# Kernel optimization log

Hardware: AMD Instinct MI355X
Metric: run time of the kernel (lower is better)

## Reference

```python
import jax, jax.numpy as jnp
import numpy as np

HW = 24       # image_size // patch_size
HEAD = 16     # vision num_attention_heads
B, T, C, H = 8, 8, 1024, 4096


def _sincos_1d(d, pos):
    omega = np.arange(d // 2, dtype=np.float32) / (d / 2.0)
    omega = 1.0 / 10000 ** omega
    out = np.einsum('m,d->md', pos.reshape(-1).astype(np.float32), omega)
    return np.concatenate([np.sin(out), np.cos(out)], axis=1)


def _pos_embed_3d(embed_dim, grid_size, t_size):
    ds = embed_dim // 4 * 3
    dt = embed_dim // 4
    gh = np.arange(grid_size, dtype=np.float32)
    grid = np.stack(np.meshgrid(gh, gh), axis=0).reshape(2, -1)  # (w, h) order as in source
    spatial = np.concatenate([_sincos_1d(ds // 2, grid[0]), _sincos_1d(ds // 2, grid[1])], axis=1)  # [g*g, ds]
    temporal = _sincos_1d(dt, np.arange(t_size, dtype=np.float32))  # [t, dt]
    spatial = np.repeat(spatial[np.newaxis], t_size, axis=0)                 # [t, g*g, ds]
    temporal = np.repeat(temporal[:, np.newaxis], grid_size ** 2, axis=1)    # [t, g*g, dt]
    emb = np.concatenate([temporal, spatial], axis=-1)
    return emb.reshape(1, t_size * grid_size ** 2, embed_dim).astype(np.float32)


def setup_inputs() -> dict:
    key = jax.random.key(0)
    k1, k2, k3 = jax.random.split(key, 3)
    x = jax.random.normal(k1, (B, T * HW * HW, C), dtype=jnp.float32)
    W1 = jax.random.normal(k2, (C, H), dtype=jnp.float32) * 0.02
    b1 = jnp.zeros((H,), jnp.float32)
    W2 = jax.random.normal(k3, (H, H), dtype=jnp.float32) * 0.02
    b2 = jnp.zeros((H,), jnp.float32)
    pos_embed = jnp.asarray(_pos_embed_3d(C, HW, T))
    return {"x": x, "pos_embed": pos_embed, "W1": W1, "b1": b1, "W2": W2, "b2": b2,
            "local_num_frames": T}


def _merge(x, unm_idx, src_idx, dst_idx):
    # ToMe merge: gather unmatched src tokens, scatter-add matched src into dst.
    src, dst = x[:, ::2], x[:, 1::2]
    unm = jnp.take_along_axis(src, unm_idx[:, :, None], axis=1)   # [b, t1-r, c]
    sel = jnp.take_along_axis(src, src_idx[:, :, None], axis=1)   # [b, r, c]
    dst = jax.vmap(lambda d, i, s: d.at[i].add(s))(dst, dst_idx, sel)
    return jnp.concatenate([unm, dst], axis=1)


def _merge_tokens(x, target, head):
    b, p, c = x.shape
    # static merge schedule (same logic as torch merge_tokens)
    rs, tmp = [], p
    while tmp != target:
        if tmp - target <= tmp // 2:
            rs.append(tmp - target)
            break
        rs.append(tmp // 2)
        tmp -= tmp // 2
    dim = c // head
    size = jnp.ones((b, p, 1), x.dtype)
    for r in rs:
        bb, pp, _ = x.shape
        # metric/index computation is under no_grad in the original
        metric = jax.lax.stop_gradient(x).reshape(bb, pp, head, dim).mean(2)
        metric = metric / jnp.linalg.norm(metric, axis=-1, keepdims=True)
        a_m, b_m = metric[:, ::2], metric[:, 1::2]
        scores = jnp.einsum('bic,bjc->bij', a_m, b_m)  # [b, ta, tb]
        node_max = scores.max(-1)
        node_idx = scores.argmax(-1)
        edge_idx = jnp.argsort(-node_max, axis=-1)      # descending
        unm_idx, src_idx = edge_idx[:, r:], edge_idx[:, :r]
        dst_idx = jnp.take_along_axis(node_idx, src_idx, axis=1)
        # weighted-average merge (merge_wavg)
        x = _merge(x * size, unm_idx, src_idx, dst_idx)
        size = _merge(size, unm_idx, src_idx, dst_idx)
        x = x / size
    return x


def reference(x, pos_embed, W1, b1, W2, b2, local_num_frames):
    x = x + pos_embed.astype(x.dtype)
    x = _merge_tokens(x, local_num_frames * 16, HEAD)
    h = jax.nn.gelu(x @ W1 + b1, approximate=False)  # nn.GELU() is exact erf gelu
    return h @ W2 + b2
```

## Files before the change

kernel.cpp:

```cpp
#include <hip/hip_runtime.h>
#include <hip/hip_bf16.h>
#include <math.h>
#include <stdint.h>

typedef unsigned short u16;
typedef __attribute__((ext_vector_type(8))) short short8;
typedef __attribute__((ext_vector_type(4))) float floatx4;

#define NB 8
#define P0 4608
#define C0 1024
#define H0 4096

__global__ void detect_mode_kernel(const uint32_t* __restrict__ pe_words, int* __restrict__ mode) {
  *mode = (pe_words[64] != 0u) ? 1 : 0;
}

__device__ __forceinline__ float load_in(const void* p, size_t idx, int mode) {
  if (mode) return __bfloat162float(((const __hip_bfloat16*)p)[idx]);
  return ((const float*)p)[idx];
}

__device__ __forceinline__ float4 load4(const void* p, size_t idx, int mode) {
  float4 r;
  if (mode) {
    ushort4 u = *(const ushort4*)((const u16*)p + idx);
    r.x = __bfloat162float(*(__hip_bfloat16*)&u.x);
    r.y = __bfloat162float(*(__hip_bfloat16*)&u.y);
    r.z = __bfloat162float(*(__hip_bfloat16*)&u.z);
    r.w = __bfloat162float(*(__hip_bfloat16*)&u.w);
  } else {
    r = *(const float4*)((const float*)p + idx);
  }
  return r;
}

__device__ __forceinline__ void write_hilo(u16* __restrict__ m2, size_t tok, int lane, float v) {
  __hip_bfloat16 hi = __float2bfloat16(v);
  float hif = __bfloat162float(hi);
  __hip_bfloat16 lo = __float2bfloat16(v - hif);
  m2[tok * 128 + lane] = *(u16*)&hi;
  m2[tok * 128 + 64 + lane] = *(u16*)&lo;
}

__global__ void metric_in_kernel(const void* __restrict__ x, const void* __restrict__ pos,
                                 const int* __restrict__ mode, u16* __restrict__ m2) {
  int tok = blockIdx.x * 4 + (threadIdx.x >> 6);
  int lane = threadIdx.x & 63;
  if (tok >= NB * P0) return;
  int b = tok / P0, t = tok - b * P0;
  int md = *mode;
  size_t xbase = ((size_t)b * P0 + t) * C0 + lane;
  size_t pbase = (size_t)t * C0 + lane;
  float s = 0.f;
  if (md) {
    const __hip_bfloat16* xp = (const __hip_bfloat16*)x + xbase;
    const __hip_bfloat16* pp = (const __hip_bfloat16*)pos + pbase;
#pragma unroll
    for (int h = 0; h < 16; ++h)
      s += __bfloat162float(xp[h * 64]) + __bfloat162float(pp[h * 64]);
  } else {
    const float* xp = (const float*)x + xbase;
    const float* pp = (const float*)pos + pbase;
#pragma unroll
    for (int h = 0; h < 16; ++h) s += xp[h * 64] + pp[h * 64];
  }
  s *= (1.f / 16.f);
  float sq = s * s;
#pragma unroll
  for (int off = 1; off < 64; off <<= 1) sq += __shfl_xor(sq, off, 64);
  write_hilo(m2, (size_t)tok, lane, s / sqrtf(sq));
}

__global__ __launch_bounds__(256) void score_mfma_kernel(const u16* __restrict__ M2,
                                                         int p, int p2, int jT2,
                                                         float* __restrict__ pm,
                                                         int* __restrict__ pi) {
  const int bi = blockIdx.x, ii = blockIdx.y, b = blockIdx.z;
  const int t = threadIdx.x, w = t >> 6, L = t & 63;
  const int wr = w >> 1, wc = w & 1;
  const int fr = L & 15, fo = (L >> 4) * 8;
  const u16* Mb = M2 + (size_t)b * p * 128;

  floatx4 acc[4][4];
#pragma unroll
  for (int mt = 0; mt < 4; ++mt)
#pragma unroll
    for (int nt = 0; nt < 4; ++nt) acc[mt][nt] = (floatx4){0.f, 0.f, 0.f, 0.f};

  const u16* arp[4];
  const u16* brp[4];
#pragma unroll
  for (int mt = 0; mt < 4; ++mt) {
    int i = ii * 128 + wr * 64 + mt * 16 + fr;
    int ta = 2 * i;
    if (ta > p - 2) ta = p - 2;
    arp[mt] = Mb + (size_t)ta * 128 + fo;
    int j = bi * 128 + wc * 64 + mt * 16 + fr;
    int tb = 2 * j + 1;
    if (tb > p - 1) tb = p - 1;
    brp[mt] = Mb + (size_t)tb * 128 + fo;
  }

#pragma unroll
  for (int ks = 0; ks < 2; ++ks) {
    short8 ah[4], al[4], bh[4], bl[4];
#pragma unroll
    for (int mt = 0; mt < 4; ++mt) {
      ah[mt] = *(const short8*)(arp[mt] + ks * 32);
      al[mt] = *(const short8*)(arp[mt] + ks * 32 + 64);
      bh[mt] = *(const short8*)(brp[mt] + ks * 32);
      bl[mt] = *(const short8*)(brp[mt] + ks * 32 + 64);
    }
#pragma unroll
    for (int mt = 0; mt < 4; ++mt)
#pragma unroll
      for (int nt = 0; nt < 4; ++nt) {
        acc[mt][nt] = __builtin_amdgcn_mfma_f32_16x16x32_bf16(ah[mt], bh[nt], acc[mt][nt], 0, 0, 0);
        acc[mt][nt] = __builtin_amdgcn_mfma_f32_16x16x32_bf16(ah[mt], bl[nt], acc[mt][nt], 0, 0, 0);
        acc[mt][nt] = __builtin_amdgcn_mfma_f32_16x16x32_bf16(al[mt], bh[nt], acc[mt][nt], 0, 0, 0);
        acc[mt][nt] = __builtin_amdgcn_mfma_f32_16x16x32_bf16(al[mt], bl[nt], acc[mt][nt], 0, 0, 0);
      }
  }

  const int gi4 = (L >> 4) * 4;
#pragma unroll
  for (int mt = 0; mt < 4; ++mt) {
#pragma unroll
    for (int reg = 0; reg < 4; ++reg) {
      int i = ii * 128 + wr * 64 + mt * 16 + gi4 + reg;
      float bm = -INFINITY;
      int bj = 0x7fffffff;
#pragma unroll
      for (int nt = 0; nt < 4; ++nt) {
        int j = bi * 128 + wc * 64 + nt * 16 + fr;
        float v = acc[mt][nt][reg];
        if (j < p2 && v > bm) { bm = v; bj = j; }
      }
#pragma unroll
      for (int mk = 1; mk < 16; mk <<= 1) {
        float om = __shfl_xor(bm, mk, 64);
        int oj = __shfl_xor(bj, mk, 64);
        if (om > bm || (om == bm && oj < bj)) { bm = om; bj = oj; }
      }
      if (fr == 0 && i < p2) {
        size_t o = ((size_t)b * 2304 + i) * jT2 + bi * 2 + wc;
        pm[o] = bm;
        pi[o] = bj;
      }
    }
  }
}

__global__ void argmax_combine_kernel(const float* __restrict__ pm, const int* __restrict__ pi,
                                      int p2, int jT, float* __restrict__ nmax,
                                      int* __restrict__ nidx, int* __restrict__ head,
                                      int* __restrict__ nxt) {
  int g = blockIdx.x * 256 + threadIdx.x;
  if (g >= NB * p2) return;
  int b = g / p2, i = g - b * p2;
  const float* r = pm + ((size_t)b * 2304 + i) * jT;
  const int* ri = pi + ((size_t)b * 2304 + i) * jT;
  float best = r[0];
  int bidx = ri[0];
  for (int k = 1; k < jT; ++k) {
    if (r[k] > best || (r[k] == best && ri[k] < bidx)) { best = r[k]; bidx = ri[k]; }
  }
  nmax[g] = best;
  nidx[g] = bidx;
  int d = bidx;
  if ((unsigned)d >= (unsigned)p2) d = 0;
  nxt[g] = atomicExch(&head[(size_t)b * p2 + d], i);
}

__global__ void init_heads_kernel(int* __restrict__ h, int n) {
  int g = blockIdx.x * 256 + threadIdx.x;
  if (g < n) h[g] = -1;
}

__global__ __launch_bounds__(256) void merge_gather_in(const void* __restrict__ x,
                                                       const void* __restrict__ pos,
                                                       const int* __restrict__ mode,
                                                       const int* __restrict__ head,
                                                       const int* __restrict__ nxt,
                                                       float* __restrict__ xo,
                                                       float* __restrict__ so, int p2,
                                                       u16* __restrict__ m2out) {
  int tj = blockIdx.x;
  int b = tj / p2, j = tj - b * p2;
  int c = threadIdx.x * 4;
  int md = *mode;
  __shared__ int sl[64];
  __shared__ int s_n, s_cur;
  __shared__ float mred[16][64];
  size_t xb = ((size_t)b * P0 + 2 * j + 1) * C0 + c;
  size_t pb = (size_t)(2 * j + 1) * C0 + c;
  float4 xa = load4(x, xb, md), pa = load4(pos, pb, md);
  float4 acc = {xa.x + pa.x, xa.y + pa.y, xa.z + pa.z, xa.w + pa.w};
  float cnt = 1.f;
  if (threadIdx.x == 0) s_cur = head[tj];
  __syncthreads();
  int cur = s_cur;
  while (cur != -1) {
    if (threadIdx.x == 0) {
      int n = 0, cc = cur;
      while (cc != -1 && n < 64) {
        sl[n++] = cc;
        cc = nxt[(size_t)b * p2 + cc];
      }
      s_n = n;
      s_cur = cc;
    }
    __syncthreads();
    int n = s_n;
    cur = s_cur;
    for (int k = 0; k < n; ++k) {
      int i = sl[k];
      size_t exb = ((size_t)b * P0 + 2 * i) * C0 + c;
      size_t epb = (size_t)(2 * i) * C0 + c;
      float4 ea = load4(x, exb, md), ep = load4(pos, epb, md);
      acc.x += ea.x + ep.x;
      acc.y += ea.y + ep.y;
      acc.z += ea.z + ep.z;
      acc.w += ea.w + ep.w;
      cnt += 1.f;
    }
    __syncthreads();
  }
  float inv = 1.f / cnt;
  float4 o = {acc.x * inv, acc.y * inv, acc.z * inv, acc.w * inv};
  *(float4*)(xo + (size_t)tj * C0 + c) = o;
  if (threadIdx.x == 0) so[tj] = cnt;
  {
    int hq = threadIdx.x >> 4, dq = (threadIdx.x & 15) * 4;
    mred[hq][dq + 0] = o.x;
    mred[hq][dq + 1] = o.y;
    mred[hq][dq + 2] = o.z;
    mred[hq][dq + 3] = o.w;
  }
  __syncthreads();
  if (threadIdx.x < 64) {
    float s = 0.f;
#pragma unroll
    for (int h = 0; h < 16; ++h) s += mred[h][threadIdx.x];
    s *= (1.f / 16.f);
    float sq = s * s;
#pragma unroll
    for (int off = 1; off < 64; off <<= 1) sq += __shfl_xor(sq, off, 64);
    write_hilo(m2out, (size_t)tj, threadIdx.x, s / sqrtf(sq));
  }
}

__global__ __launch_bounds__(256) void merge_gather_f(const float* __restrict__ xi,
                                                      const float* __restrict__ si,
                                                      const int* __restrict__ head,
                                                      const int* __restrict__ nxt,
                                                      float* __restrict__ xo,
                                                      float* __restrict__ so, int p, int p2,
                                                      u16* __restrict__ m2out) {
  int tj = blockIdx.x;
  int b = tj / p2, j = tj - b * p2;
  int c = threadIdx.x * 4;
  __shared__ int sl[64];
  __shared__ int s_n, s_cur;
  __shared__ float mred[16][64];
  float sz = si[(size_t)b * p + 2 * j + 1];
  float4 v = *(const float4*)(xi + ((size_t)b * p + 2 * j + 1) * C0 + c);
  float4 acc = {v.x * sz, v.y * sz, v.z * sz, v.w * sz};
  float ssum = sz;
  if (threadIdx.x == 0) s_cur = head[tj];
  __syncthreads();
  int cur = s_cur;
  while (cur != -1) {
    if (threadIdx.x == 0) {
      int n = 0, cc = cur;
      while (cc != -1 && n < 64) {
        sl[n++] = cc;
        cc = nxt[(size_t)b * p2 + cc];
      }
      s_n = n;
      s_cur = cc;
    }
    __syncthreads();
    int n = s_n;
    cur = s_cur;
    for (int k = 0; k < n; ++k) {
      int i = sl[k];
      float szi = si[(size_t)b * p + 2 * i];
      float4 e = *(const float4*)(xi + ((size_t)b * p + 2 * i) * C0 + c);
      acc.x += e.x * szi;
      acc.y += e.y * szi;
      acc.z += e.z * szi;
      acc.w += e.w * szi;
      ssum += szi;
    }
    __syncthreads();
  }
  float inv = 1.f / ssum;
  float4 o = {acc.x * inv, acc.y * inv, acc.z * inv, acc.w * inv};
  *(float4*)(xo + (size_t)tj * C0 + c) = o;
  if (threadIdx.x == 0) so[tj] = ssum;
  {
    int hq = threadIdx.x >> 4, dq = (threadIdx.x & 15) * 4;
    mred[hq][dq + 0] = o.x;
    mred[hq][dq + 1] = o.y;
    mred[hq][dq + 2] = o.z;
    mred[hq][dq + 3] = o.w;
  }
  __syncthreads();
  if (threadIdx.x < 64) {
    float s = 0.f;
#pragma unroll
    for (int h = 0; h < 16; ++h) s += mred[h][threadIdx.x];
    s *= (1.f / 16.f);
    float sq = s * s;
#pragma unroll
    for (int off = 1; off < 64; off <<= 1) sq += __shfl_xor(sq, off, 64);
    write_hilo(m2out, (size_t)tj, threadIdx.x, s / sqrtf(sq));
  }
}

__global__ void rank_kernel(const float* __restrict__ nmax, const int* __restrict__ nidx,
                            int* __restrict__ unm_map, int* __restrict__ src_ord,
                            int* __restrict__ src_dst) {
  int b = blockIdx.x;
  int i = threadIdx.x;
  __shared__ float v[72];
  __shared__ int nx[72];
  if (i < 72) { v[i] = nmax[b * 72 + i]; nx[i] = nidx[b * 72 + i]; }
  __syncthreads();
  if (i < 72) {
    float vi = v[i];
    int rank = 0;
    for (int k = 0; k < 72; ++k) {
      float vk = v[k];
      rank += (vk > vi) || (vk == vi && k < i);
    }
    if (rank < 16) {
      int d = nx[i];
      if ((unsigned)d >= 72u) d = 0;
      src_ord[b * 16 + rank] = i;
      src_dst[b * 16 + rank] = d;
    } else {
      unm_map[b * 56 + (rank - 16)] = i;
    }
  }
}

__global__ void final_init(const float* __restrict__ x5, const float* __restrict__ s5,
                           const int* __restrict__ unm_map, float* __restrict__ xf,
                           float* __restrict__ sf) {
  int bt = blockIdx.x;
  int b = bt >> 7, tk = bt & 127;
  int c = threadIdx.x * 4;
  float4 o;
  float szo;
  if (tk < 56) {
    int se = unm_map[b * 56 + tk];
    if ((unsigned)se >= 72u) se = 0;
    o = *(const float4*)(x5 + ((size_t)b * 144 + 2 * se) * C0 + c);
    szo = 1.f;
  } else {
    int j = tk - 56;
    float sz = s5[b * 144 + 2 * j + 1];
    float4 v = *(const float4*)(x5 + ((size_t)b * 144 + 2 * j + 1) * C0 + c);
    o.x = v.x * sz; o.y = v.y * sz; o.z = v.z * sz; o.w = v.w * sz;
    szo = sz;
  }
  *(float4*)(xf + (size_t)bt * C0 + c) = o;
  if (threadIdx.x == 0) sf[bt] = szo;
}

__global__ void final_scatter(const float* __restrict__ x5, const float* __restrict__ s5,
                              const int* __restrict__ src_ord, const int* __restrict__ src_dst,
                              float* __restrict__ xf, float* __restrict__ sf) {
  int bk = blockIdx.x;
  int b = bk >> 4, k = bk & 15;
  int c = threadIdx.x * 4;
  int st = src_ord[b * 16 + k], dst = src_dst[b * 16 + k];
  if ((unsigned)st >= 72u) st = 0;
  if ((unsigned)dst >= 72u) dst = 0;
  float sz = s5[b * 144 + 2 * st];
  float4 v = *(const float4*)(x5 + ((size_t)b * 144 + 2 * st) * C0 + c);
  float* out = xf + ((size_t)(b * 128 + 56 + dst)) * C0 + c;
  atomicAdd(out + 0, v.x * sz);
  atomicAdd(out + 1, v.y * sz);
  atomicAdd(out + 2, v.z * sz);
  atomicAdd(out + 3, v.w * sz);
  if (threadIdx.x == 0) atomicAdd(sf + b * 128 + 56 + dst, sz);
}

__global__ void final_div_cvt(const float* __restrict__ xf, const float* __restrict__ sf,
                              __hip_bfloat16* __restrict__ xb) {
  int bt = blockIdx.x;
  int c = threadIdx.x * 4;
  float sz = sf[bt];
  float4 v = *(const float4*)(xf + (size_t)bt * C0 + c);
  __hip_bfloat16* o = xb + (size_t)bt * C0 + c;
  o[0] = __float2bfloat16(v.x / sz);
  o[1] = __float2bfloat16(v.y / sz);
  o[2] = __float2bfloat16(v.z / sz);
  o[3] = __float2bfloat16(v.w / sz);
}

__global__ void transpose_in(const void* __restrict__ in, const int* __restrict__ mode,
                             u16* __restrict__ out, int K, int N) {
  __shared__ u16 tile[64][65];
  int n0 = blockIdx.x * 64, k0 = blockIdx.y * 64;
  int t = threadIdx.x;
  int md = *mode;
  int r = t >> 4, c4 = (t & 15) * 4;
  if (md) {
#pragma unroll
    for (int pass = 0; pass < 4; ++pass) {
      int row = r + pass * 16;
      ushort4 u = *(const ushort4*)((const u16*)in + (size_t)(k0 + row) * N + n0 + c4);
      tile[row][c4 + 0] = u.x;
      tile[row][c4 + 1] = u.y;
      tile[row][c4 + 2] = u.z;
      tile[row][c4 + 3] = u.w;
    }
  } else {
#pragma unroll
    for (int pass = 0; pass < 4; ++pass) {
      int row = r + pass * 16;
      float4 v = *(const float4*)((const float*)in + (size_t)(k0 + row) * N + n0 + c4);
      __hip_bfloat16 b0 = __float2bfloat16(v.x), b1 = __float2bfloat16(v.y);
      __hip_bfloat16 b2 = __float2bfloat16(v.z), b3 = __float2bfloat16(v.w);
      tile[row][c4 + 0] = *(u16*)&b0;
      tile[row][c4 + 1] = *(u16*)&b1;
      tile[row][c4 + 2] = *(u16*)&b2;
      tile[row][c4 + 3] = *(u16*)&b3;
    }
  }
  __syncthreads();
#pragma unroll
  for (int pass = 0; pass < 4; ++pass) {
    int row = r + pass * 16;
    ushort4 o;
    o.x = tile[c4][row]; o.y = tile[c4 + 1][row]; o.z = tile[c4 + 2][row]; o.w = tile[c4 + 3][row];
    *(ushort4*)(out + (size_t)(n0 + row) * K + k0 + c4) = o;
  }
}

#define GL2LDS(gp, lp)                                                                   \
  __builtin_amdgcn_global_load_lds((const __attribute__((address_space(1))) uint32_t*)(gp), \
                                   (__attribute__((address_space(3))) uint32_t*)(lp), 16, 0, 0)

__global__ __launch_bounds__(256, 2) void gemm_bt(const u16* __restrict__ A,
                                                  const u16* __restrict__ BT,
                                                  const void* __restrict__ bias,
                                                  const int* __restrict__ mode,
                                                  void* __restrict__ C, int M, int N,
                                                  int K, int act, int out_sel) {
  __shared__ __align__(16) u16 As[2 * 64 * 64];
  __shared__ __align__(16) u16 Bs[2 * 128 * 64];
  const int t = threadIdx.x, w = t >> 6, L = t & 63;
  const int m0 = blockIdx.y * 64, n0 = blockIdx.x * 128;
  const int wr = w >> 1, wc = w & 1;
  const int md = *mode;
  const int fr = L & 15;
  floatx4 acc[2][4];
#pragma unroll
  for (int a = 0; a < 2; ++a)
#pragma unroll
    for (int bb = 0; bb < 4; ++bb) acc[a][bb] = (floatx4){0.f, 0.f, 0.f, 0.f};

  auto stage = [&](int buf, int kk) {
#pragma unroll
    for (int q = 0; q < 2; ++q) {
      int g = q * 256 + t;
      int row = g >> 3, colg = (g & 7) ^ (row & 7);
      GL2LDS(A + (size_t)(m0 + row) * K + kk + colg * 8, As + buf * 4096 + g * 8);
    }
#pragma unroll
    for (int q = 0; q < 4; ++q) {
      int g = q * 256 + t;
      int row = g >> 3, colg = (g & 7) ^ (row & 7);
      GL2LDS(BT + (size_t)(n0 + row) * K + kk + colg * 8, Bs + buf * 8192 + g * 8);
    }
  };

  stage(0, 0);
  const int NT = K >> 6;
  int cur = 0;
  for (int it = 0; it < NT; ++it) {
    if (it + 1 < NT) {
      stage(cur ^ 1, (it + 1) << 6);
      asm volatile("s_waitcnt vmcnt(6)" ::: "memory");
    } else {
      asm volatile("s_waitcnt vmcnt(0)" ::: "memory");
    }
    __builtin_amdgcn_s_barrier();
    const u16* Ab = As + cur * 4096;
    const u16* Bb = Bs + cur * 8192;
    __builtin_amdgcn_s_setprio(1);
#pragma unroll
    for (int kh = 0; kh < 2; ++kh) {
      short8 af[2], bfr[4];
#pragma unroll
      for (int mt = 0; mt < 2; ++mt) {
        int ra = wr * 32 + mt * 16 + fr;
        int cg = (kh * 4 + (L >> 4)) ^ (ra & 7);
        af[mt] = *(const short8*)(Ab + ra * 64 + cg * 8);
      }
#pragma unroll
      for (int nt = 0; nt < 4; ++nt) {
        int rb = wc * 64 + nt * 16 + fr;
        int cg = (kh * 4 + (L >> 4)) ^ (rb & 7);
        bfr[nt] = *(const short8*)(Bb + rb * 64 + cg * 8);
      }
#pragma unroll
      for (int mt = 0; mt < 2; ++mt)
#pragma unroll
        for (int nt = 0; nt < 4; ++nt)
          acc[mt][nt] =
              __builtin_amdgcn_mfma_f32_16x16x32_bf16(af[mt], bfr[nt], acc[mt][nt], 0, 0, 0);
    }
    __builtin_amdgcn_s_setprio(0);
    __builtin_amdgcn_s_barrier();
    cur ^= 1;
  }
  const int gi4 = (L >> 4) * 4;
#pragma unroll
  for (int mt = 0; mt < 2; ++mt)
#pragma unroll
    for (int nt = 0; nt < 4; ++nt) {
      int n = n0 + wc * 64 + nt * 16 + fr;
      float bz = load_in(bias, n, md);
#pragma unroll
      for (int rr = 0; rr < 4; ++rr) {
        int m = m0 + wr * 32 + mt * 16 + gi4 + rr;
        float v = acc[mt][nt][rr] + bz;
        if (act) v = 0.5f * v * (1.f + erff(v * 0.70710678118654752f));
        size_t idx = (size_t)m * N + n;
        if (out_sel == 0 || md) {
          __hip_bfloat16 bv = __float2bfloat16(v);
          ((u16*)C)[idx] = *(u16*)&bv;
        } else {
          ((float*)C)[idx] = v;
        }
      }
    }
}

extern "C" void kernel_launch(void* const* d_in, const int* in_sizes, int n_in, void* d_out,
                              int out_size, void* d_ws, size_t ws_size, hipStream_t stream) {
  const void* x = d_in[0];
  const void* pe = d_in[1];
  const void* W1 = d_in[2];
  const void* b1 = d_in[3];
  const void* W2 = d_in[4];
  const void* b2 = d_in[5];

  char* base = (char*)d_ws;
  size_t off = 0;
  auto alloc = [&](size_t bytes) -> void* {
    void* p = base + off;
    off += (bytes + 255) & ~(size_t)255;
    return p;
  };
  int* mode = (int*)alloc(256);
  u16* m2 = (u16*)alloc((size_t)NB * 4608 * 128 * 2);
  float* pm = (float*)alloc((size_t)NB * 2304 * 36 * 4);
  int* pi = (int*)alloc((size_t)NB * 2304 * 36 * 4);
  float* nmax = (float*)alloc((size_t)NB * 2304 * 4);
  int* nidx = (int*)alloc((size_t)NB * 2304 * 4);
  float* bufA = (float*)alloc((size_t)NB * 2304 * C0 * 4);
  float* bufB = (float*)alloc((size_t)NB * 1152 * C0 * 4);
  float* s1 = (float*)alloc((size_t)NB * 2304 * 4);
  float* s2 = (float*)alloc((size_t)NB * 1152 * 4);
  float* s3 = (float*)alloc((size_t)NB * 576 * 4);
  float* s4 = (float*)alloc((size_t)NB * 288 * 4);
  float* s5 = (float*)alloc((size_t)NB * 144 * 4);
  float* sf = (float*)alloc((size_t)NB * 128 * 4);
  int* unm_map = (int*)alloc((size_t)NB * 56 * 4);
  int* src_ord = (int*)alloc((size_t)NB * 16 * 4);
  int* src_dst = (int*)alloc((size_t)NB * 16 * 4);
  u16* xfb = (u16*)alloc((size_t)NB * 128 * C0 * 2);
  u16* hbuf = (u16*)alloc((size_t)1024 * H0 * 2);
  u16* w1t = (u16*)alloc((size_t)H0 * C0 * 2);
  u16* w2t = (u16*)alloc((size_t)H0 * H0 * 2);
  int* heads = (int*)alloc((size_t)NB * 4536 * 4);
  int* nxt = (int*)alloc((size_t)NB * 2304 * 4);
  if (off > ws_size) return;

  int* h_it[6];
  h_it[0] = heads;
  h_it[1] = h_it[0] + NB * 2304;
  h_it[2] = h_it[1] + NB * 1152;
  h_it[3] = h_it[2] + NB * 576;
  h_it[4] = h_it[3] + NB * 288;
  h_it[5] = h_it[4] + NB * 144;

  float* x1 = bufA;
  float* x2 = bufB;
  float* x3 = bufA;
  float* x4 = bufB;
  float* x5 = bufA;
  float* xf = bufB;

  detect_mode_kernel<<<1, 1, 0, stream>>>((const uint32_t*)pe, mode);
  init_heads_kernel<<<(NB * 4536 + 255) / 256, 256, 0, stream>>>(heads, NB * 4536);

  transpose_in<<<dim3(4096 / 64, 1024 / 64), 256, 0, stream>>>(W1, mode, w1t, 1024, 4096);
  transpose_in<<<dim3(4096 / 64, 4096 / 64), 256, 0, stream>>>(W2, mode, w2t, 4096, 4096);

  metric_in_kernel<<<NB * P0 / 4, 256, 0, stream>>>(x, pe, mode, m2);
  score_mfma_kernel<<<dim3(18, 18, NB), 256, 0, stream>>>(m2, 4608, 2304, 36, pm, pi);
  argmax_combine_kernel<<<(NB * 2304 + 255) / 256, 256, 0, stream>>>(pm, pi, 2304, 36, nmax,
                                                                     nidx, h_it[0], nxt);
  merge_gather_in<<<NB * 2304, 256, 0, stream>>>(x, pe, mode, h_it[0], nxt, x1, s1, 2304, m2);

  float* xs_in[4] = {x1, x2, x3, x4};
  float* ss_in[4] = {s1, s2, s3, s4};
  float* xs_out[4] = {x2, x3, x4, x5};
  float* ss_out[4] = {s2, s3, s4, s5};
  int ps[5] = {2304, 1152, 576, 288, 144};
  for (int it = 0; it < 4; ++it) {
    int p = ps[it], p2 = ps[it + 1];
    int iT = (p2 + 127) / 128, jT = (p2 + 127) / 128;
    score_mfma_kernel<<<dim3(jT, iT, NB), 256, 0, stream>>>(m2, p, p2, 2 * jT, pm, pi);
    argmax_combine_kernel<<<(NB * p2 + 255) / 256, 256, 0, stream>>>(pm, pi, p2, 2 * jT, nmax,
                                                                     nidx, h_it[it + 1], nxt);
    merge_gather_f<<<NB * p2, 256, 0, stream>>>(xs_in[it], ss_in[it], h_it[it + 1], nxt,
                                                xs_out[it], ss_out[it], p, p2, m2);
  }

  score_mfma_kernel<<<dim3(1, 1, NB), 256, 0, stream>>>(m2, 144, 72, 2, pm, pi);
  argmax_combine_kernel<<<(NB * 72 + 255) / 256, 256, 0, stream>>>(pm, pi, 72, 2, nmax, nidx,
                                                                   h_it[5], nxt);
  rank_kernel<<<NB, 128, 0, stream>>>(nmax, nidx, unm_map, src_ord, src_dst);
  final_init<<<NB * 128, 256, 0, stream>>>(x5, s5, unm_map, xf, sf);
  final_scatter<<<NB * 16, 256, 0, stream>>>(x5, s5, src_ord, src_dst, xf, sf);
  final_div_cvt<<<NB * 128, 256, 0, stream>>>(xf, sf, (__hip_bfloat16*)xfb);

  gemm_bt<<<dim3(4096 / 128, 1024 / 64), 256, 0, stream>>>(xfb, w1t, b1, mode, hbuf, 1024, 4096,
                                                           1024, 1, 0);
  gemm_bt<<<dim3(4096 / 128, 1024 / 64), 256, 0, stream>>>(hbuf, w2t, b2, mode, d_out, 1024,
                                                           4096, 4096, 0, 1);
}
```

Before: 754.6 us.

## Fuse tail kernels, vectorize metric loads, triple-buffer GEMM pipeline

Folds the mode detection into the head-init kernel, and merges the final argmax with ranking. It also replaces the init/atomic-scatter/divide/convert sequence with a single gather kernel that writes bf16 directly, cutting launch count and atomics. The metric kernel now uses float4 loads with a shuffle reduction instead of strided scalar loads. The GEMM moves from double to triple-buffered LDS staging with a deeper prefetch, which raises shared-memory use and may lower occupancy.

```diff
diff --git a/kernel.cpp b/kernel.cpp
--- a/kernel.cpp
+++ b/kernel.cpp
@@ -11,10 +11,6 @@
 #define P0 4608
 #define C0 1024
 #define H0 4096
-
-__global__ void detect_mode_kernel(const uint32_t* __restrict__ pe_words, int* __restrict__ mode) {
-  *mode = (pe_words[64] != 0u) ? 1 : 0;
-}
 
 __device__ __forceinline__ float load_in(const void* p, size_t idx, int mode) {
   if (mode) return __bfloat162float(((const __hip_bfloat16*)p)[idx]);
@@ -43,33 +39,68 @@
   m2[tok * 128 + 64 + lane] = *(u16*)&lo;
 }
 
+__global__ void init_heads_kernel(int* __restrict__ h, int n,
+                                  const uint32_t* __restrict__ pe_words,
+                                  int* __restrict__ mode) {
+  int g = blockIdx.x * 256 + threadIdx.x;
+  if (g < n) h[g] = -1;
+  if (g == 0) *mode = (pe_words[64] != 0u) ? 1 : 0;
+}
+
 __global__ void metric_in_kernel(const void* __restrict__ x, const void* __restrict__ pos,
                                  const int* __restrict__ mode, u16* __restrict__ m2) {
   int tok = blockIdx.x * 4 + (threadIdx.x >> 6);
-  int lane = threadIdx.x & 63;
+  int l = threadIdx.x & 63;
   if (tok >= NB * P0) return;
   int b = tok / P0, t = tok - b * P0;
   int md = *mode;
-  size_t xbase = ((size_t)b * P0 + t) * C0 + lane;
-  size_t pbase = (size_t)t * C0 + lane;
-  float s = 0.f;
+  size_t xrow = ((size_t)b * P0 + t) * C0;
+  size_t prow = (size_t)t * C0;
+  float4 acc = {0.f, 0.f, 0.f, 0.f};
   if (md) {
-    const __hip_bfloat16* xp = (const __hip_bfloat16*)x + xbase;
-    const __hip_bfloat16* pp = (const __hip_bfloat16*)pos + pbase;
-#pragma unroll
-    for (int h = 0; h < 16; ++h)
-      s += __bfloat162float(xp[h * 64]) + __bfloat162float(pp[h * 64]);
+#pragma unroll
+    for (int hp = 0; hp < 4; ++hp) {
+      float4 v = load4(x, xrow + hp * 256 + 4 * l, 1);
+      float4 w = load4(pos, prow + hp * 256 + 4 * l, 1);
+      acc.x += v.x + w.x; acc.y += v.y + w.y; acc.z += v.z + w.z; acc.w += v.w + w.w;
+    }
   } else {
-    const float* xp = (const float*)x + xbase;
-    const float* pp = (const float*)pos + pbase;
-#pragma unroll
-    for (int h = 0; h < 16; ++h) s += xp[h * 64] + pp[h * 64];
-  }
-  s *= (1.f / 16.f);
-  float sq = s * s;
-#pragma unroll
-  for (int off = 1; off < 64; off <<= 1) sq += __shfl_xor(sq, off, 64);
-  write_hilo(m2, (size_t)tok, lane, s / sqrtf(sq));
+#pragma unroll
+    for (int hp = 0; hp < 4; ++hp) {
+      float4 v = *(const float4*)((const float*)x + xrow + hp * 256 + 4 * l);
+      float4 w = *(const float4*)((const float*)pos + prow + hp * 256 + 4 * l);
+      acc.x += v.x + w.x; acc.y += v.y + w.y; acc.z += v.z + w.z; acc.w += v.w + w.w;
+    }
+  }
+#pragma unroll
+  for (int mk = 16; mk <= 32; mk <<= 1) {
+    acc.x += __shfl_xor(acc.x, mk, 64);
+    acc.y += __shfl_xor(acc.y, mk, 64);
+    acc.z += __shfl_xor(acc.z, mk, 64);
+    acc.w += __shfl_xor(acc.w, mk, 64);
+  }
+  acc.x *= (1.f / 16.f); acc.y *= (1.f / 16.f); acc.z *= (1.f / 16.f); acc.w *= (1.f / 16.f);
+  float sq = acc.x * acc.x + acc.y * acc.y + acc.z * acc.z + acc.w * acc.w;
+#pragma unroll
+  for (int mk = 1; mk <= 8; mk <<= 1) sq += __shfl_xor(sq, mk, 64);
+  if ((l >> 4) == 0) {
+    float inv = 1.f / sqrtf(sq);
+    int s4 = (l & 15) * 4;
+    ushort4 hi4, lo4;
+    float vv[4] = {acc.x * inv, acc.y * inv, acc.z * inv, acc.w * inv};
+    u16 hw[4], lw[4];
+#pragma unroll
+    for (int e = 0; e < 4; ++e) {
+      __hip_bfloat16 hi = __float2bfloat16(vv[e]);
+      float hif = __bfloat162float(hi);
+      __hip_bfloat16 lo = __float2bfloat16(vv[e] - hif);
+      hw[e] = *(u16*)&hi; lw[e] = *(u16*)&lo;
+    }
+    hi4.x = hw[0]; hi4.y = hw[1]; hi4.z = hw[2]; hi4.w = hw[3];
+    lo4.x = lw[0]; lo4.y = lw[1]; lo4.z = lw[2]; lo4.w = lw[3];
+    *(ushort4*)(m2 + (size_t)tok * 128 + s4) = hi4;
+    *(ushort4*)(m2 + (size_t)tok * 128 + 64 + s4) = lo4;
+  }
 }
 
 __global__ __launch_bounds__(256) void score_mfma_kernel(const u16* __restrict__ M2,
@@ -171,11 +202,6 @@
   int d = bidx;
   if ((unsigned)d >= (unsigned)p2) d = 0;
   nxt[g] = atomicExch(&head[(size_t)b * p2 + d], i);
-}
-
-__global__ void init_heads_kernel(int* __restrict__ h, int n) {
-  int g = blockIdx.x * 256 + threadIdx.x;
-  if (g < n) h[g] = -1;
 }
 
 __global__ __launch_bounds__(256) void merge_gather_in(const void* __restrict__ x,
@@ -320,14 +346,22 @@
   }
 }
 
-__global__ void rank_kernel(const float* __restrict__ nmax, const int* __restrict__ nidx,
-                            int* __restrict__ unm_map, int* __restrict__ src_ord,
-                            int* __restrict__ src_dst) {
+__global__ void rank_combine_kernel(const float* __restrict__ pm, const int* __restrict__ pi,
+                                    int* __restrict__ unm_map, int* __restrict__ src_ord,
+                                    int* __restrict__ src_dst) {
   int b = blockIdx.x;
   int i = threadIdx.x;
   __shared__ float v[72];
   __shared__ int nx[72];
-  if (i < 72) { v[i] = nmax[b * 72 + i]; nx[i] = nidx[b * 72 + i]; }
+  if (i < 72) {
+    const float* r = pm + ((size_t)b * 2304 + i) * 2;
+    const int* ri = pi + ((size_t)b * 2304 + i) * 2;
+    float best = r[0];
+    int bidx = ri[0];
+    if (r[1] > best || (r[1] == best && ri[1] < bidx)) { best = r[1]; bidx = ri[1]; }
+    v[i] = best;
+    nx[i] = bidx;
+  }
   __syncthreads();
   if (i < 72) {
     float vi = v[i];
@@ -347,60 +381,54 @@
   }
 }
 
-__global__ void final_init(const float* __restrict__ x5, const float* __restrict__ s5,
-                           const int* __restrict__ unm_map, float* __restrict__ xf,
-                           float* __restrict__ sf) {
+__global__ __launch_bounds__(256) void final_gather(const float* __restrict__ x5,
+                                                    const float* __restrict__ s5,
+                                                    const int* __restrict__ unm_map,
+                                                    const int* __restrict__ src_ord,
+                                                    const int* __restrict__ src_dst,
+                                                    __hip_bfloat16* __restrict__ xb) {
   int bt = blockIdx.x;
   int b = bt >> 7, tk = bt & 127;
   int c = threadIdx.x * 4;
+  __shared__ int sord[16], sdst[16];
+  if (threadIdx.x < 16) {
+    sord[threadIdx.x] = src_ord[b * 16 + threadIdx.x];
+    sdst[threadIdx.x] = src_dst[b * 16 + threadIdx.x];
+  }
+  __syncthreads();
   float4 o;
-  float szo;
   if (tk < 56) {
     int se = unm_map[b * 56 + tk];
     if ((unsigned)se >= 72u) se = 0;
     o = *(const float4*)(x5 + ((size_t)b * 144 + 2 * se) * C0 + c);
-    szo = 1.f;
   } else {
     int j = tk - 56;
     float sz = s5[b * 144 + 2 * j + 1];
     float4 v = *(const float4*)(x5 + ((size_t)b * 144 + 2 * j + 1) * C0 + c);
-    o.x = v.x * sz; o.y = v.y * sz; o.z = v.z * sz; o.w = v.w * sz;
-    szo = sz;
-  }
-  *(float4*)(xf + (size_t)bt * C0 + c) = o;
-  if (threadIdx.x == 0) sf[bt] = szo;
-}
-
-__global__ void final_scatter(const float* __restrict__ x5, const float* __restrict__ s5,
-                              const int* __restrict__ src_ord, const int* __restrict__ src_dst,
-                              float* __restrict__ xf, float* __restrict__ sf) {
-  int bk = blockIdx.x;
-  int b = bk >> 4, k = bk & 15;
-  int c = threadIdx.x * 4;
-  int st = src_ord[b * 16 + k], dst = src_dst[b * 16 + k];
-  if ((unsigned)st >= 72u) st = 0;
-  if ((unsigned)dst >= 72u) dst = 0;
-  float sz = s5[b * 144 + 2 * st];
-  float4 v = *(const float4*)(x5 + ((size_t)b * 144 + 2 * st) * C0 + c);
-  float* out = xf + ((size_t)(b * 128 + 56 + dst)) * C0 + c;
-  atomicAdd(out + 0, v.x * sz);
-  atomicAdd(out + 1, v.y * sz);
-  atomicAdd(out + 2, v.z * sz);
-  atomicAdd(out + 3, v.w * sz);
-  if (threadIdx.x == 0) atomicAdd(sf + b * 128 + 56 + dst, sz);
-}
-
-__global__ void final_div_cvt(const float* __restrict__ xf, const float* __restrict__ sf,
-                              __hip_bfloat16* __restrict__ xb) {
-  int bt = blockIdx.x;
-  int c = threadIdx.x * 4;
-  float sz = sf[bt];
-  float4 v = *(const float4*)(xf + (size_t)bt * C0 + c);
-  __hip_bfloat16* o = xb + (size_t)bt * C0 + c;
-  o[0] = __float2bfloat16(v.x / sz);
-  o[1] = __float2bfloat16(v.y / sz);
-  o[2] = __float2bfloat16(v.z / sz);
-  o[3] = __float2bfloat16(v.w / sz);
+    float4 acc = {v.x * sz, v.y * sz, v.z * sz, v.w * sz};
+    float ssum = sz;
+#pragma unroll
+    for (int k = 0; k < 16; ++k) {
+      if (sdst[k] == j) {
+        int st = sord[k];
+        if ((unsigned)st >= 72u) st = 0;
+        float szi = s5[b * 144 + 2 * st];
+        float4 e = *(const float4*)(x5 + ((size_t)b * 144 + 2 * st) * C0 + c);
+        acc.x += e.x * szi;
+        acc.y += e.y * szi;
+        acc.z += e.z * szi;
+        acc.w += e.w * szi;
+        ssum += szi;
+      }
+    }
+    float inv = 1.f / ssum;
+    o.x = acc.x * inv; o.y = acc.y * inv; o.z = acc.z * inv; o.w = acc.w * inv;
+  }
+  __hip_bfloat16* op = xb + (size_t)bt * C0 + c;
+  op[0] = __float2bfloat16(o.x);
+  op[1] = __float2bfloat16(o.y);
+  op[2] = __float2bfloat16(o.z);
+  op[3] = __float2bfloat16(o.w);
 }
 
 __global__ void transpose_in(const void* __restrict__ in, const int* __restrict__ mode,
@@ -453,8 +481,8 @@
                                                   const int* __restrict__ mode,
                                                   void* __restrict__ C, int M, int N,
                                                   int K, int act, int out_sel) {
-  __shared__ __align__(16) u16 As[2 * 64 * 64];
-  __shared__ __align__(16) u16 Bs[2 * 128 * 64];
+  __shared__ __align__(16) u16 As[3 * 64 * 64];
+  __shared__ __align__(16) u16 Bs[3 * 128 * 64];
   const int t = threadIdx.x, w = t >> 6, L = t & 63;
   const int m0 = blockIdx.y * 64, n0 = blockIdx.x * 128;
   const int wr = w >> 1, wc = w & 1;
@@ -481,12 +509,17 @@
     }
   };
 
+  const int NT = K >> 6;
   stage(0, 0);
-  const int NT = K >> 6;
+  stage(1, 64);
   int cur = 0;
   for (int it = 0; it < NT; ++it) {
-    if (it + 1 < NT) {
-      stage(cur ^ 1, (it + 1) << 6);
+    if (it + 2 < NT) {
+      int b2 = cur + 2;
+      if (b2 >= 3) b2 -= 3;
+      stage(b2, (it + 2) << 6);
+      asm volatile("s_waitcnt vmcnt(12)" ::: "memory");
+    } else if (it + 1 < NT) {
       asm volatile("s_waitcnt vmcnt(6)" ::: "memory");
     } else {
       asm volatile("s_waitcnt vmcnt(0)" ::: "memory");
@@ -519,7 +552,7 @@
     }
     __builtin_amdgcn_s_setprio(0);
     __builtin_amdgcn_s_barrier();
-    cur ^= 1;
+    cur = (cur + 1 == 3) ? 0 : cur + 1;
   }
   const int gi4 = (L >> 4) * 4;
 #pragma unroll
@@ -573,7 +606,6 @@
   float* s3 = (float*)alloc((size_t)NB * 576 * 4);
   float* s4 = (float*)alloc((size_t)NB * 288 * 4);
   float* s5 = (float*)alloc((size_t)NB * 144 * 4);
-  float* sf = (float*)alloc((size_t)NB * 128 * 4);
   int* unm_map = (int*)alloc((size_t)NB * 56 * 4);
   int* src_ord = (int*)alloc((size_t)NB * 16 * 4);
   int* src_dst = (int*)alloc((size_t)NB * 16 * 4);
@@ -581,27 +613,25 @@
   u16* hbuf = (u16*)alloc((size_t)1024 * H0 * 2);
   u16* w1t = (u16*)alloc((size_t)H0 * C0 * 2);
   u16* w2t = (u16*)alloc((size_t)H0 * H0 * 2);
-  int* heads = (int*)alloc((size_t)NB * 4536 * 4);
+  int* heads = (int*)alloc((size_t)NB * 4464 * 4);
   int* nxt = (int*)alloc((size_t)NB * 2304 * 4);
   if (off > ws_size) return;
 
-  int* h_it[6];
+  int* h_it[5];
   h_it[0] = heads;
   h_it[1] = h_it[0] + NB * 2304;
   h_it[2] = h_it[1] + NB * 1152;
   h_it[3] = h_it[2] + NB * 576;
   h_it[4] = h_it[3] + NB * 288;
-  h_it[5] = h_it[4] + NB * 144;
 
   float* x1 = bufA;
   float* x2 = bufB;
   float* x3 = bufA;
   float* x4 = bufB;
   float* x5 = bufA;
-  float* xf = bufB;
-
-  detect_mode_kernel<<<1, 1, 0, stream>>>((const uint32_t*)pe, mode);
-  init_heads_kernel<<<(NB * 4536 + 255) / 256, 256, 0, stream>>>(heads, NB * 4536);
+
+  init_heads_kernel<<<(NB * 4464 + 255) / 256, 256, 0, stream>>>(heads, NB * 4464,
+                                                                 (const uint32_t*)pe, mode);
 
   transpose_in<<<dim3(4096 / 64, 1024 / 64), 256, 0, stream>>>(W1, mode, w1t, 1024, 4096);
   transpose_in<<<dim3(4096 / 64, 4096 / 64), 256, 0, stream>>>(W2, mode, w2t, 4096, 4096);
@@ -628,12 +658,9 @@
   }
 
   score_mfma_kernel<<<dim3(1, 1, NB), 256, 0, stream>>>(m2, 144, 72, 2, pm, pi);
-  argmax_combine_kernel<<<(NB * 72 + 255) / 256, 256, 0, stream>>>(pm, pi, 72, 2, nmax, nidx,
-                                                                   h_it[5], nxt);
-  rank_kernel<<<NB, 128, 0, stream>>>(nmax, nidx, unm_map, src_ord, src_dst);
-  final_init<<<NB * 128, 256, 0, stream>>>(x5, s5, unm_map, xf, sf);
-  final_scatter<<<NB * 16, 256, 0, stream>>>(x5, s5, src_ord, src_dst, xf, sf);
-  final_div_cvt<<<NB * 128, 256, 0, stream>>>(xf, sf, (__hip_bfloat16*)xfb);
+  rank_combine_kernel<<<NB, 128, 0, stream>>>(pm, pi, unm_map, src_ord, src_dst);
+  final_gather<<<NB * 128, 256, 0, stream>>>(x5, s5, unm_map, src_ord, src_dst,
+                                             (__hip_bfloat16*)xfb);
 
   gemm_bt<<<dim3(4096 / 128, 1024 / 64), 256, 0, stream>>>(xfb, w1t, b1, mode, hbuf, 1024, 4096,
                                                            1024, 1, 0);
```

After: 742.3 us. Within noise of the previous version (-1.6%).
